# Kernel optimization log

Hardware: AMD Instinct MI355X
Metric: run time of the kernel (lower is better)

## Reference

```python
import jax, jax.numpy as jnp
import numpy as np

N, D, H, E, K = 4096, 512, 2048, 8, 2  # tokens, input/output dim, expert hidden, num_experts, top_k


def setup_inputs() -> dict:
    key = jax.random.key(0)
    k_x, k_r, k_w1, k_b1, k_w2, k_b2 = jax.random.split(key, 6)
    input_batch = jax.random.normal(k_x, (N, D), dtype=jnp.float32)
    # Router-style top-k selection: guarantees the K expert ids per token are distinct
    # (required by the torch nonzero-based dispatch) and probabilities are a softmax
    # over the selected logits, matching a standard MoE sampler.
    router_logits = jax.random.normal(k_r, (N, E), dtype=jnp.float32)
    top_vals, top_idx = jax.lax.top_k(router_logits, K)
    probabilities = jax.nn.softmax(top_vals, axis=-1)            # [N, K]
    indices = top_idx.astype(jnp.int64)                          # [N, K]
    scale = 0.02
    W1 = scale * jax.random.normal(k_w1, (E, D, H), dtype=jnp.float32)
    b1 = jnp.zeros((E, H), dtype=jnp.float32)
    W2 = scale * jax.random.normal(k_w2, (E, H, D), dtype=jnp.float32)
    b2 = jnp.zeros((E, D), dtype=jnp.float32)
    return {"input_batch": input_batch, "probabilities": probabilities, "indices": indices,
            "W1": W1, "b1": b1, "W2": W2, "b2": b2}


def reference(input_batch, probabilities, indices, W1, b1, W2, b2):
    # Each expert is a dense 2-layer GELU MLP. The torch module gathers the tokens
    # assigned to each expert, runs the expert, concatenates, sorts back to original
    # flattened [N*K] order, applies probability weighting AFTER the experts, then
    # reshapes to [N, K, D] and sums over K. That is mathematically:
    #   out[t] = sum_k probabilities[t, k] * expert_{indices[t, k]}(input_batch[t])
    h = jax.nn.gelu(jnp.einsum('nd,edh->enh', input_batch, W1) + b1[:, None, :])  # [E, N, H]
    y = jnp.einsum('enh,ehd->end', h, W2) + b2[:, None, :]                         # [E, N, D]
    y = jnp.transpose(y, (1, 0, 2))                                                # [N, E, D]
    sel = jnp.take_along_axis(y, indices[:, :, None], axis=1)                      # [N, K, D]
    output = jnp.sum(sel * probabilities[:, :, None], axis=1)                      # [N, D]
    total_loss = jnp.float32(0.0)  # no sampler / expert aux losses in this config
    return output, total_loss
```

## Files before the change

kernel.cpp:

```cpp
#include <hip/hip_runtime.h>
#include <cstdint>
#include <cstddef>

#define NTOK 4096
#define DIMD 512
#define HIDH 2048
#define NEXP 8
#define TOPK 2
#define NSLOT (NTOK*TOPK)
#define SLACK 256
#define YROWS (NSLOT+SLACK)

#define BK 64

typedef short bf16x8_t __attribute__((ext_vector_type(8)));
typedef float f32x4_t  __attribute__((ext_vector_type(4)));

__device__ __forceinline__ unsigned short f2b(float f){
  unsigned int x = __float_as_uint(f);
  unsigned int r = (x + 0x7FFFu + ((x >> 16) & 1u)) >> 16;
  return (unsigned short)r;
}

__device__ __forceinline__ float gelu_tanh(float x) {
  float z2 = 1.5957691216057308f * fmaf(0.044715f * x, x * x, x);
  return x / (1.f + __expf(-z2));
}

__device__ __forceinline__ void gl_lds16(const void* g, void* l){
  __builtin_amdgcn_global_load_lds((const __attribute__((address_space(1))) void*)g,
                                   (__attribute__((address_space(3))) void*)l, 16, 0, 0);
}


__global__ __launch_bounds__(256) void cvt_x(const float* __restrict__ x, unsigned short* __restrict__ xb){
  int i = blockIdx.x*256 + threadIdx.x;
  if (i >= (NTOK*DIMD)/4) return;
  float4 v = ((const float4*)x)[i];
  ushort4 o; o.x=f2b(v.x); o.y=f2b(v.y); o.z=f2b(v.z); o.w=f2b(v.w);
  ((ushort4*)xb)[i] = o;
}

__global__ __launch_bounds__(256) void transpose_cvt(const float* __restrict__ src,
                                                     unsigned short* __restrict__ dst,
                                                     int R, int C){
  int e = blockIdx.z;
  src += (size_t)e*R*C; dst += (size_t)e*R*C;
  int c0 = blockIdx.x*64, r0 = blockIdx.y*64;
  __shared__ float t[64][65];
  int tr = threadIdx.x >> 4, tc = threadIdx.x & 15;
  #pragma unroll
  for (int i=0;i<4;i++){
    int r = tr + i*16;
    float4 v = *(const float4*)(src + (size_t)(r0 + r)*C + c0 + tc*4);
    t[r][tc*4+0]=v.x; t[r][tc*4+1]=v.y; t[r][tc*4+2]=v.z; t[r][tc*4+3]=v.w;
  }
  __syncthreads();
  #pragma unroll
  for (int i=0;i<4;i++){
    int c = tr + i*16;
    ushort4 o;
    o.x = f2b(t[tc*4+0][c]); o.y = f2b(t[tc*4+1][c]);
    o.z = f2b(t[tc*4+2][c]); o.w = f2b(t[tc*4+3][c]);
    *(ushort4*)(dst + (size_t)(c0 + c)*R + r0 + tc*4) = o;
  }
}


__global__ void count_k(const int* __restrict__ I, int* __restrict__ meta){
  int i = blockIdx.x*256+threadIdx.x;
  if (i < NSLOT) atomicAdd(&meta[I[i]], 1);
}
__global__ void scan_k(int* __restrict__ meta){
  if (threadIdx.x==0 && blockIdx.x==0){
    int s=0;
    for(int e=0;e<NEXP;e++){ meta[16+e]=s; s+=meta[e]; }
  }
}
__global__ void fill_k(const int* __restrict__ I, int* __restrict__ meta,
                       int* __restrict__ tokOf, int* __restrict__ rowOf){
  int i = blockIdx.x*256+threadIdx.x;
  if (i < NSLOT){
    int e = I[i];
    int pos = meta[16+e] + atomicAdd(&meta[8+e], 1);
    tokOf[pos] = i >> 1;
    rowOf[i] = pos;
  }
}



__global__ __launch_bounds__(512,1) void gemm1(
    const unsigned short* __restrict__ Xb, const unsigned short* __restrict__ W1t,
    const float* __restrict__ B1, const int* __restrict__ meta,
    const int* __restrict__ tokOf, unsigned short* __restrict__ H)
{
  const int e = blockIdx.z;
  const int cnt = meta[e];
  const int row0 = blockIdx.y * 256;
  if (row0 >= cnt) return;
  const int off = meta[16+e];
  const int h0 = blockIdx.x * 256;

  extern __shared__ unsigned short sm[];

  const int tid = threadIdx.x;
  const int tr  = tid >> 3;
  const int csw = ((tid & 7) ^ (tr & 7)) << 3;

  const unsigned short* sA[4];
  const unsigned short* sB[4];
  #pragma unroll
  for (int i=0;i<4;i++){
    int slot = min(off + row0 + i*64 + tr, NSLOT-1);
    sA[i] = Xb  + (size_t)tokOf[slot]*DIMD + csw;
    sB[i] = W1t + ((size_t)e*HIDH + h0 + i*64 + tr)*DIMD + csw;
  }

  const int lane = tid & 63, wid = tid >> 6;
  const int wrM = (wid >> 2) * 128, wcN = (wid & 3) * 64;
  const int l15 = lane & 15, kg = lane >> 4;
  const int lx  = l15 & 7;
  int rowA[8], rowB[4];
  #pragma unroll
  for (int m=0;m<8;m++) rowA[m] = (wrM + m*16 + l15) * BK;
  #pragma unroll
  for (int n=0;n<4;n++) rowB[n] = (wcN + n*16 + l15) * BK;
  const int ch0 = ((kg    ) ^ lx) << 3;
  const int ch1 = ((kg + 4) ^ lx) << 3;

  f32x4_t acc[8][4];
  #pragma unroll
  for (int m=0;m<8;m++){
    #pragma unroll
    for (int n=0;n<4;n++) acc[m][n] = (f32x4_t){0.f,0.f,0.f,0.f};
  }

  auto stagef = [&](int buf, int kt){
    unsigned short* dA = sm + buf*32768 + tid*8;
    unsigned short* dB = dA + 16384;
    const int k0 = kt * BK;
    #pragma unroll
    for (int i=0;i<4;i++){
      gl_lds16(sA[i] + k0, dA + i*4096);
      gl_lds16(sB[i] + k0, dB + i*4096);
    }
  };

  auto khalf = [&](const unsigned short* SA, const unsigned short* SB, int ch){
    bf16x8_t bfr[4];
    #pragma unroll
    for (int n=0;n<4;n++) bfr[n] = *(const bf16x8_t*)&SB[rowB[n] + ch];
    #pragma unroll
    for (int m=0;m<8;m++){
      bf16x8_t afm = *(const bf16x8_t*)&SA[rowA[m] + ch];
      #pragma unroll
      for (int n=0;n<4;n++)
        acc[m][n] = __builtin_amdgcn_mfma_f32_16x16x32_bf16(afm, bfr[n], acc[m][n], 0,0,0);
    }
  };

  constexpr int NS = DIMD / BK;
  stagef(0, 0);
  for (int t = 0; t < NS; ++t){
    const int cur = t & 1;
    if (t + 1 < NS){
      stagef(cur ^ 1, t + 1);
      asm volatile("s_waitcnt vmcnt(8)" ::: "memory");
    } else {
      asm volatile("s_waitcnt vmcnt(0)" ::: "memory");
    }
    __builtin_amdgcn_s_barrier();
    __builtin_amdgcn_s_setprio(1);
    const unsigned short* SA = sm + cur*32768;
    const unsigned short* SB = SA + 16384;
    khalf(SA, SB, ch0);
    khalf(SA, SB, ch1);
    __builtin_amdgcn_s_setprio(0);
    __builtin_amdgcn_s_barrier();
  }

  const int r4 = kg * 4;
  #pragma unroll
  for (int n=0;n<4;n++){
    const int gcol = h0 + wcN + n*16 + l15;
    const float b1v = B1[(size_t)e*HIDH + gcol];
    #pragma unroll
    for (int m=0;m<8;m++){
      const int rbase = row0 + wrM + m*16 + r4;
      #pragma unroll
      for (int r=0;r<4;r++){
        const int row = rbase + r;
        if (row < cnt)
          H[(size_t)(off + row)*HIDH + gcol] = f2b(gelu_tanh(acc[m][n][r] + b1v));
      }
    }
  }
}


__global__ __launch_bounds__(512,1) void gemm2(
    const unsigned short* __restrict__ Hb, const unsigned short* __restrict__ W2t,
    const int* __restrict__ meta, float* __restrict__ Y, int nsplit)
{
  const int e = blockIdx.z;
  const int cnt = meta[e];
  const int row0 = blockIdx.y * 256;
  if (row0 >= cnt) return;
  const int off = meta[16+e];
  const int ncol = DIMD / 256;
  const int d0 = (blockIdx.x % ncol) * 256;
  const int kc = blockIdx.x / ncol;
  const int kchunk = HIDH / nsplit;
  const int kbase = kc * kchunk;
  const int NS = kchunk / BK;

  extern __shared__ unsigned short sm[];

  const int tid = threadIdx.x;
  const int tr  = tid >> 3;
  const int csw = ((tid & 7) ^ (tr & 7)) << 3;

  const unsigned short* sA[4];
  const unsigned short* sB[4];
  #pragma unroll
  for (int i=0;i<4;i++){
    int arow = min(off + row0 + i*64 + tr, YROWS-1);
    sA[i] = Hb  + (size_t)arow*HIDH + kbase + csw;
    sB[i] = W2t + ((size_t)e*DIMD + d0 + i*64 + tr)*HIDH + kbase + csw;
  }

  const int lane = tid & 63, wid = tid >> 6;
  const int wrM = (wid >> 2) * 128, wcN = (wid & 3) * 64;
  const int l15 = lane & 15, kg = lane >> 4;
  const int lx  = l15 & 7;
  int rowA[8], rowB[4];
  #pragma unroll
  for (int m=0;m<8;m++) rowA[m] = (wrM + m*16 + l15) * BK;
  #pragma unroll
  for (int n=0;n<4;n++) rowB[n] = (wcN + n*16 + l15) * BK;
  const int ch0 = ((kg    ) ^ lx) << 3;
  const int ch1 = ((kg + 4) ^ lx) << 3;

  f32x4_t acc[8][4];
  #pragma unroll
  for (int m=0;m<8;m++){
    #pragma unroll
    for (int n=0;n<4;n++) acc[m][n] = (f32x4_t){0.f,0.f,0.f,0.f};
  }

  auto stagef = [&](int buf, int kt){
    unsigned short* dA = sm + buf*32768 + tid*8;
    unsigned short* dB = dA + 16384;
    const int k0 = kt * BK;
    #pragma unroll
    for (int i=0;i<4;i++){
      gl_lds16(sA[i] + k0, dA + i*4096);
      gl_lds16(sB[i] + k0, dB + i*4096);
    }
  };

  auto khalf = [&](const unsigned short* SA, const unsigned short* SB, int ch){
    bf16x8_t bfr[4];
    #pragma unroll
    for (int n=0;n<4;n++) bfr[n] = *(const bf16x8_t*)&SB[rowB[n] + ch];
    #pragma unroll
    for (int m=0;m<8;m++){
      bf16x8_t afm = *(const bf16x8_t*)&SA[rowA[m] + ch];
      #pragma unroll
      for (int n=0;n<4;n++)
        acc[m][n] = __builtin_amdgcn_mfma_f32_16x16x32_bf16(afm, bfr[n], acc[m][n], 0,0,0);
    }
  };

  stagef(0, 0);
  for (int t = 0; t < NS; ++t){
    const int cur = t & 1;
    if (t + 1 < NS){
      stagef(cur ^ 1, t + 1);
      asm volatile("s_waitcnt vmcnt(8)" ::: "memory");
    } else {
      asm volatile("s_waitcnt vmcnt(0)" ::: "memory");
    }
    __builtin_amdgcn_s_barrier();
    __builtin_amdgcn_s_setprio(1);
    const unsigned short* SA = sm + cur*32768;
    const unsigned short* SB = SA + 16384;
    khalf(SA, SB, ch0);
    khalf(SA, SB, ch1);
    __builtin_amdgcn_s_setprio(0);
    __builtin_amdgcn_s_barrier();
  }

  float* Yp = Y + (size_t)kc * YROWS * DIMD;
  const int r4 = kg * 4;
  #pragma unroll
  for (int m=0;m<8;m++){
    const int rbase = row0 + wrM + m*16 + r4;
    #pragma unroll
    for (int r=0;r<4;r++){
      const int row = rbase + r;
      if (row < cnt){
        float* yp = Yp + (size_t)(off + row)*DIMD + d0 + wcN + l15;
        #pragma unroll
        for (int n=0;n<4;n++) yp[n*16] = acc[m][n][r];
      }
    }
  }
}


__global__ __launch_bounds__(128) void reduce_k(
    const float* __restrict__ P, const int* __restrict__ I, const int* __restrict__ rowOf,
    const float* __restrict__ Y, const float* __restrict__ B2, float* __restrict__ out,
    int nsplit)
{
  int t = blockIdx.x; int d4 = threadIdx.x;
  float4 a = make_float4(0.f,0.f,0.f,0.f);
  #pragma unroll
  for (int k=0;k<TOPK;k++){
    int i = t*TOPK + k;
    float p = P[i]; int e = I[i]; int r = rowOf[i];
    float4 b = *(const float4*)(B2 + (size_t)e*DIMD + d4*4);
    float4 y = make_float4(b.x, b.y, b.z, b.w);
    for (int c=0;c<nsplit;c++){
      float4 v = *(const float4*)(Y + (size_t)c*YROWS*DIMD + (size_t)r*DIMD + d4*4);
      y.x += v.x; y.y += v.y; y.z += v.z; y.w += v.w;
    }
    a.x = fmaf(p, y.x, a.x); a.y = fmaf(p, y.y, a.y);
    a.z = fmaf(p, y.z, a.z); a.w = fmaf(p, y.w, a.w);
  }
  *(float4*)(out + (size_t)t*DIMD + d4*4) = a;
}


#define CAP (NTOK*TOPK)
#define ROWS 32
#define HC 64
#define NTHR 256
#define XS_LD 516
#define HS_LD 36

__global__ void fb_build(const int* __restrict__ idx, const float* __restrict__ probs,
                         int* __restrict__ counts, int* __restrict__ tok,
                         float* __restrict__ pr) {
    int i = blockIdx.x * blockDim.x + threadIdx.x;
    if (i >= NTOK * TOPK) return;
    int t = i / TOPK;
    int e = idx[i];
    float p = probs[i];
    int pos = atomicAdd(&counts[e], 1);
    tok[e * CAP + pos] = t;
    pr[e * CAP + pos] = p;
}

__global__ __launch_bounds__(NTHR)
void fb_moe(const float* __restrict__ X,
            const float* __restrict__ W1, const float* __restrict__ B1,
            const float* __restrict__ W2, const float* __restrict__ B2,
            const int* __restrict__ counts, const int* __restrict__ tok,
            const float* __restrict__ pr, float* __restrict__ out)
{
    const int e = blockIdx.y;
    const int cnt = counts[e];
    const int r0 = blockIdx.x * ROWS;
    if (r0 >= cnt) return;
    const int nr = min(ROWS, cnt - r0);

    extern __shared__ float smem[];
    float* Xs = smem;
    float* Hs = smem + ROWS * XS_LD;
    const int tid = threadIdx.x;

    for (int i = tid; i < ROWS * (DIMD / 4); i += NTHR) {
        int r = i >> 7;
        int c4 = i & 127;
        float4 v = make_float4(0.f, 0.f, 0.f, 0.f);
        if (r < nr) {
            int t = tok[e * CAP + r0 + r];
            v = *(const float4*)(X + (size_t)t * DIMD + c4 * 4);
        }
        *(float4*)(Xs + r * XS_LD + c4 * 4) = v;
    }
    __syncthreads();

    const int hq = tid & 15;
    const int rp = tid >> 4;
    const int wv = tid >> 6;
    const int ln = tid & 63;

    float yacc[8][8];
    #pragma unroll
    for (int r = 0; r < 8; ++r){
        #pragma unroll
        for (int c = 0; c < 8; ++c) yacc[r][c] = 0.f;
    }

    const float* w1base = W1 + (size_t)e * DIMD * HIDH;
    const float* w2base = W2 + (size_t)e * HIDH * DIMD;
    const float* b1base = B1 + e * HIDH;

    for (int h0 = 0; h0 < HIDH; h0 += HC) {
        float acc0[4] = {0.f, 0.f, 0.f, 0.f};
        float acc1[4] = {0.f, 0.f, 0.f, 0.f};
        const float* w1p = w1base + h0 + hq * 4;
        const float* xr0 = Xs + (rp * 2) * XS_LD;
        const float* xr1 = xr0 + XS_LD;
        #pragma unroll 2
        for (int d = 0; d < DIMD; d += 4) {
            float4 xa = *(const float4*)(xr0 + d);
            float4 xb = *(const float4*)(xr1 + d);
            float4 w0 = *(const float4*)(w1p + (size_t)(d + 0) * HIDH);
            float4 w1v = *(const float4*)(w1p + (size_t)(d + 1) * HIDH);
            float4 w2v = *(const float4*)(w1p + (size_t)(d + 2) * HIDH);
            float4 w3v = *(const float4*)(w1p + (size_t)(d + 3) * HIDH);
            float xav[4] = {xa.x, xa.y, xa.z, xa.w};
            float xbv[4] = {xb.x, xb.y, xb.z, xb.w};
            float4 wsv[4] = {w0, w1v, w2v, w3v};
            #pragma unroll
            for (int dd = 0; dd < 4; ++dd) {
                acc0[0] = fmaf(xav[dd], wsv[dd].x, acc0[0]);
                acc0[1] = fmaf(xav[dd], wsv[dd].y, acc0[1]);
                acc0[2] = fmaf(xav[dd], wsv[dd].z, acc0[2]);
                acc0[3] = fmaf(xav[dd], wsv[dd].w, acc0[3]);
                acc1[0] = fmaf(xbv[dd], wsv[dd].x, acc1[0]);
                acc1[1] = fmaf(xbv[dd], wsv[dd].y, acc1[1]);
                acc1[2] = fmaf(xbv[dd], wsv[dd].z, acc1[2]);
                acc1[3] = fmaf(xbv[dd], wsv[dd].w, acc1[3]);
            }
        }
        {
            float4 b1v = *(const float4*)(b1base + h0 + hq * 4);
            float bb[4] = {b1v.x, b1v.y, b1v.z, b1v.w};
            #pragma unroll
            for (int j = 0; j < 4; ++j) {
                Hs[(hq * 4 + j) * HS_LD + rp * 2]     = gelu_tanh(acc0[j] + bb[j]);
                Hs[(hq * 4 + j) * HS_LD + rp * 2 + 1] = gelu_tanh(acc1[j] + bb[j]);
            }
        }
        __syncthreads();

        const float* w2p = w2base + (size_t)h0 * DIMD;
        #pragma unroll 4
        for (int hc = 0; hc < HC; ++hc) {
            float4 wA = *(const float4*)(w2p + (size_t)hc * DIMD + ln * 4);
            float4 wB = *(const float4*)(w2p + (size_t)hc * DIMD + 256 + ln * 4);
            float4 hv0 = *(const float4*)(Hs + hc * HS_LD + wv * 8);
            float4 hv1 = *(const float4*)(Hs + hc * HS_LD + wv * 8 + 4);
            float hr[8] = {hv0.x, hv0.y, hv0.z, hv0.w, hv1.x, hv1.y, hv1.z, hv1.w};
            #pragma unroll
            for (int r = 0; r < 8; ++r) {
                yacc[r][0] = fmaf(hr[r], wA.x, yacc[r][0]);
                yacc[r][1] = fmaf(hr[r], wA.y, yacc[r][1]);
                yacc[r][2] = fmaf(hr[r], wA.z, yacc[r][2]);
                yacc[r][3] = fmaf(hr[r], wA.w, yacc[r][3]);
                yacc[r][4] = fmaf(hr[r], wB.x, yacc[r][4]);
                yacc[r][5] = fmaf(hr[r], wB.y, yacc[r][5]);
                yacc[r][6] = fmaf(hr[r], wB.z, yacc[r][6]);
                yacc[r][7] = fmaf(hr[r], wB.w, yacc[r][7]);
            }
        }
        __syncthreads();
    }

    const float* b2p = B2 + e * DIMD;
    float4 b2A = *(const float4*)(b2p + ln * 4);
    float4 b2B = *(const float4*)(b2p + 256 + ln * 4);
    float bA[4] = {b2A.x, b2A.y, b2A.z, b2A.w};
    float bB[4] = {b2B.x, b2B.y, b2B.z, b2B.w};
    #pragma unroll
    for (int r = 0; r < 8; ++r) {
        int rg = wv * 8 + r;
        if (rg < nr) {
            int t = tok[e * CAP + r0 + rg];
            float p = pr[e * CAP + r0 + rg];
            float* op = out + (size_t)t * DIMD;
            #pragma unroll
            for (int j = 0; j < 4; ++j) {
                atomicAdd(op + ln * 4 + j,        p * (yacc[r][j] + bA[j]));
                atomicAdd(op + 256 + ln * 4 + j,  p * (yacc[r][4 + j] + bB[j]));
            }
        }
    }
}


extern "C" void kernel_launch(void* const* d_in, const int* in_sizes, int n_in,
                              void* d_out, int out_size, void* d_ws, size_t ws_size,
                              hipStream_t stream) {
    const float* X  = (const float*)d_in[0];
    const float* P  = (const float*)d_in[1];
    const int*   I  = (const int*)d_in[2];
    const float* W1 = (const float*)d_in[3];
    const float* B1 = (const float*)d_in[4];
    const float* W2 = (const float*)d_in[5];
    const float* B2 = (const float*)d_in[6];
    float* out = (float*)d_out;
    char* ws = (char*)d_ws;

    int nsplit = 0;
    size_t o_meta=0, o_tok=0, o_row=0, o_xb=0, o_w1t=0, o_w2t=0, o_h=0, o_y=0;
    const int cand[3] = {4, 2, 1};
    for (int ci = 0; ci < 3; ++ci) {
        int ns = cand[ci];
        size_t cur = 0;
        auto alloc = [&](size_t b){ size_t p = cur; cur += (b + 255) & ~(size_t)255; return p; };
        size_t m_ = alloc(256);
        size_t t_ = alloc((size_t)NSLOT*4);
        size_t r_ = alloc((size_t)NSLOT*4);
        size_t x_ = alloc((size_t)NTOK*DIMD*2);
        size_t w1_ = alloc((size_t)NEXP*DIMD*HIDH*2);
        size_t w2_ = alloc((size_t)NEXP*DIMD*HIDH*2);
        size_t h_ = alloc((size_t)YROWS*HIDH*2);
        size_t y_ = alloc((size_t)ns*YROWS*DIMD*4);
        if (cur <= ws_size) {
            nsplit = ns;
            o_meta=m_; o_tok=t_; o_row=r_; o_xb=x_; o_w1t=w1_; o_w2t=w2_; o_h=h_; o_y=y_;
            break;
        }
    }

    if (nsplit > 0) {
        int* meta = (int*)(ws + o_meta);
        int* tokOf = (int*)(ws + o_tok);
        int* rowOf = (int*)(ws + o_row);
        unsigned short* Xb  = (unsigned short*)(ws + o_xb);
        unsigned short* W1t = (unsigned short*)(ws + o_w1t);
        unsigned short* W2t = (unsigned short*)(ws + o_w2t);
        unsigned short* Hb  = (unsigned short*)(ws + o_h);
        float* Yb = (float*)(ws + o_y);

        hipMemsetAsync(meta, 0, 256, stream);
        cvt_x<<<(NTOK*DIMD/4 + 255)/256, 256, 0, stream>>>(X, Xb);
        transpose_cvt<<<dim3(HIDH/64, DIMD/64, NEXP), 256, 0, stream>>>(W1, W1t, DIMD, HIDH);
        transpose_cvt<<<dim3(DIMD/64, HIDH/64, NEXP), 256, 0, stream>>>(W2, W2t, HIDH, DIMD);
        count_k<<<NSLOT/256, 256, 0, stream>>>(I, meta);
        scan_k<<<1, 64, 0, stream>>>(meta);
        fill_k<<<NSLOT/256, 256, 0, stream>>>(I, meta, tokOf, rowOf);

        hipFuncSetAttribute((const void*)gemm1,
                            hipFuncAttributeMaxDynamicSharedMemorySize, 131072);
        hipFuncSetAttribute((const void*)gemm2,
                            hipFuncAttributeMaxDynamicSharedMemorySize, 131072);
        gemm1<<<dim3(HIDH/256, NSLOT/256, NEXP), 512, 131072, stream>>>(
            Xb, W1t, B1, meta, tokOf, Hb);
        gemm2<<<dim3((DIMD/256)*nsplit, NSLOT/256, NEXP), 512, 131072, stream>>>(
            Hb, W2t, meta, Yb, nsplit);
        reduce_k<<<NTOK, 128, 0, stream>>>(P, I, rowOf, Yb, B2, out, nsplit);
    } else {
        int*   counts = (int*)ws;
        int*   tok    = (int*)(ws + 64);
        float* pr     = (float*)(ws + 64 + (size_t)NEXP * CAP * sizeof(int));

        hipMemsetAsync(counts, 0, NEXP * sizeof(int), stream);
        hipMemsetAsync(d_out, 0, (size_t)out_size * sizeof(float), stream);
        fb_build<<<(NTOK * TOPK + 255) / 256, 256, 0, stream>>>(I, P, counts, tok, pr);
        size_t smem = (size_t)(ROWS * XS_LD + HC * HS_LD) * sizeof(float);
        hipFuncSetAttribute((const void*)fb_moe,
                            hipFuncAttributeMaxDynamicSharedMemorySize, (int)smem);
        fb_moe<<<dim3(CAP / ROWS, NEXP), NTHR, smem, stream>>>(
            X, W1, B1, W2, B2, counts, tok, pr, out);
    }
}
```

Measured before the change: 231.7 us.

## Shrink grouped GEMM tiles to 128x128 with 256 threads and two blocks per CU

Both expert GEMMs move from 256x256 tiles with 512 threads and one block per CU to 128x128 tiles with 256 threads, four waves and two blocks per CU, halving shared memory per block. The hand-tuned vmcnt waits, setprio hints and split barriers are replaced by a plain double-buffered loop with __syncthreads. The goal is more blocks and less padding waste on ragged per-expert row counts, plus better occupancy. In exchange each tile reuses loaded data less, and the simpler synchronisation may expose load latency.

Result: faster. 203.5 us (-12.2%).

```diff
diff --git a/kernel.cpp b/kernel.cpp
--- a/kernel.cpp
+++ b/kernel.cpp
@@ -11,7 +11,7 @@
 #define SLACK 256
 #define YROWS (NSLOT+SLACK)
 
-#define BK 64
+#define BK2 64
 
 typedef short bf16x8_t __attribute__((ext_vector_type(8)));
 typedef float f32x4_t  __attribute__((ext_vector_type(4)));
@@ -90,17 +90,17 @@
 
 
 
-__global__ __launch_bounds__(512,1) void gemm1(
+__global__ __launch_bounds__(256,2) void gemm1(
     const unsigned short* __restrict__ Xb, const unsigned short* __restrict__ W1t,
     const float* __restrict__ B1, const int* __restrict__ meta,
     const int* __restrict__ tokOf, unsigned short* __restrict__ H)
 {
   const int e = blockIdx.z;
   const int cnt = meta[e];
-  const int row0 = blockIdx.y * 256;
+  const int row0 = blockIdx.y * 128;
   if (row0 >= cnt) return;
   const int off = meta[16+e];
-  const int h0 = blockIdx.x * 256;
+  const int h0 = blockIdx.x * 128;
 
   extern __shared__ unsigned short sm[];
 
@@ -112,82 +112,76 @@
   const unsigned short* sB[4];
   #pragma unroll
   for (int i=0;i<4;i++){
-    int slot = min(off + row0 + i*64 + tr, NSLOT-1);
+    int slot = min(off + row0 + i*32 + tr, NSLOT-1);
     sA[i] = Xb  + (size_t)tokOf[slot]*DIMD + csw;
-    sB[i] = W1t + ((size_t)e*HIDH + h0 + i*64 + tr)*DIMD + csw;
+    sB[i] = W1t + ((size_t)e*HIDH + h0 + i*32 + tr)*DIMD + csw;
   }
 
   const int lane = tid & 63, wid = tid >> 6;
-  const int wrM = (wid >> 2) * 128, wcN = (wid & 3) * 64;
+  const int wr = (wid >> 1) * 64, wc = (wid & 1) * 64;
   const int l15 = lane & 15, kg = lane >> 4;
-  const int lx  = l15 & 7;
-  int rowA[8], rowB[4];
-  #pragma unroll
-  for (int m=0;m<8;m++) rowA[m] = (wrM + m*16 + l15) * BK;
-  #pragma unroll
-  for (int n=0;n<4;n++) rowB[n] = (wcN + n*16 + l15) * BK;
-  const int ch0 = ((kg    ) ^ lx) << 3;
-  const int ch1 = ((kg + 4) ^ lx) << 3;
-
-  f32x4_t acc[8][4];
-  #pragma unroll
-  for (int m=0;m<8;m++){
-    #pragma unroll
-    for (int n=0;n<4;n++) acc[m][n] = (f32x4_t){0.f,0.f,0.f,0.f};
-  }
-
-  auto stagef = [&](int buf, int kt){
-    unsigned short* dA = sm + buf*32768 + tid*8;
-    unsigned short* dB = dA + 16384;
-    const int k0 = kt * BK;
+  int rowA[4], rowB[4];
+  #pragma unroll
+  for (int m=0;m<4;m++) rowA[m] = (wr + m*16 + l15) * BK2;
+  #pragma unroll
+  for (int n=0;n<4;n++) rowB[n] = (wc + n*16 + l15) * BK2;
+  const int ch0 = ((kg    ) ^ (l15 & 7)) << 3;
+  const int ch1 = ((kg + 4) ^ (l15 & 7)) << 3;
+
+  f32x4_t acc[4][4];
+  #pragma unroll
+  for (int i=0;i<4;i++){
+    #pragma unroll
+    for (int j=0;j<4;j++) acc[i][j] = (f32x4_t){0.f,0.f,0.f,0.f};
+  }
+
+  auto stage = [&](int buf, int kt){
+    unsigned short* d = sm + buf*16384 + tid*8;
+    const int k0 = kt * BK2;
     #pragma unroll
     for (int i=0;i<4;i++){
-      gl_lds16(sA[i] + k0, dA + i*4096);
-      gl_lds16(sB[i] + k0, dB + i*4096);
+      gl_lds16(sA[i] + k0, d + i*2048);
+      gl_lds16(sB[i] + k0, d + 8192 + i*2048);
     }
   };
 
-  auto khalf = [&](const unsigned short* SA, const unsigned short* SB, int ch){
-    bf16x8_t bfr[4];
-    #pragma unroll
-    for (int n=0;n<4;n++) bfr[n] = *(const bf16x8_t*)&SB[rowB[n] + ch];
-    #pragma unroll
-    for (int m=0;m<8;m++){
-      bf16x8_t afm = *(const bf16x8_t*)&SA[rowA[m] + ch];
-      #pragma unroll
-      for (int n=0;n<4;n++)
-        acc[m][n] = __builtin_amdgcn_mfma_f32_16x16x32_bf16(afm, bfr[n], acc[m][n], 0,0,0);
+  auto compute = [&](int buf){
+    const unsigned short* SA = sm + buf*16384;
+    const unsigned short* SB = SA + 8192;
+    #pragma unroll
+    for (int h=0; h<2; ++h){
+      const int ch = h ? ch1 : ch0;
+      bf16x8_t bfr[4], af[4];
+      #pragma unroll
+      for (int n=0;n<4;n++) bfr[n] = *(const bf16x8_t*)&SB[rowB[n] + ch];
+      #pragma unroll
+      for (int m=0;m<4;m++) af[m]  = *(const bf16x8_t*)&SA[rowA[m] + ch];
+      #pragma unroll
+      for (int m=0;m<4;m++){
+        #pragma unroll
+        for (int n=0;n<4;n++)
+          acc[m][n] = __builtin_amdgcn_mfma_f32_16x16x32_bf16(af[m], bfr[n], acc[m][n], 0,0,0);
+      }
     }
   };
 
-  constexpr int NS = DIMD / BK;
-  stagef(0, 0);
+  constexpr int NS = DIMD / BK2;
+  stage(0, 0);
+  __syncthreads();
   for (int t = 0; t < NS; ++t){
-    const int cur = t & 1;
-    if (t + 1 < NS){
-      stagef(cur ^ 1, t + 1);
-      asm volatile("s_waitcnt vmcnt(8)" ::: "memory");
-    } else {
-      asm volatile("s_waitcnt vmcnt(0)" ::: "memory");
-    }
-    __builtin_amdgcn_s_barrier();
-    __builtin_amdgcn_s_setprio(1);
-    const unsigned short* SA = sm + cur*32768;
-    const unsigned short* SB = SA + 16384;
-    khalf(SA, SB, ch0);
-    khalf(SA, SB, ch1);
-    __builtin_amdgcn_s_setprio(0);
-    __builtin_amdgcn_s_barrier();
+    if (t + 1 < NS) stage((t+1) & 1, t+1);
+    compute(t & 1);
+    __syncthreads();
   }
 
   const int r4 = kg * 4;
   #pragma unroll
   for (int n=0;n<4;n++){
-    const int gcol = h0 + wcN + n*16 + l15;
+    const int gcol = h0 + wc + n*16 + l15;
     const float b1v = B1[(size_t)e*HIDH + gcol];
     #pragma unroll
-    for (int m=0;m<8;m++){
-      const int rbase = row0 + wrM + m*16 + r4;
+    for (int m=0;m<4;m++){
+      const int rbase = row0 + wr + m*16 + r4;
       #pragma unroll
       for (int r=0;r<4;r++){
         const int row = rbase + r;
@@ -199,21 +193,21 @@
 }
 
 
-__global__ __launch_bounds__(512,1) void gemm2(
+__global__ __launch_bounds__(256,2) void gemm2(
     const unsigned short* __restrict__ Hb, const unsigned short* __restrict__ W2t,
     const int* __restrict__ meta, float* __restrict__ Y, int nsplit)
 {
   const int e = blockIdx.z;
   const int cnt = meta[e];
-  const int row0 = blockIdx.y * 256;
+  const int row0 = blockIdx.y * 128;
   if (row0 >= cnt) return;
   const int off = meta[16+e];
-  const int ncol = DIMD / 256;
-  const int d0 = (blockIdx.x % ncol) * 256;
+  const int ncol = DIMD / 128;
+  const int d0 = (blockIdx.x % ncol) * 128;
   const int kc = blockIdx.x / ncol;
   const int kchunk = HIDH / nsplit;
   const int kbase = kc * kchunk;
-  const int NS = kchunk / BK;
+  const int NS = kchunk / BK2;
 
   extern __shared__ unsigned short sm[];
 
@@ -225,83 +219,77 @@
   const unsigned short* sB[4];
   #pragma unroll
   for (int i=0;i<4;i++){
-    int arow = min(off + row0 + i*64 + tr, YROWS-1);
+    int arow = min(off + row0 + i*32 + tr, YROWS-1);
     sA[i] = Hb  + (size_t)arow*HIDH + kbase + csw;
-    sB[i] = W2t + ((size_t)e*DIMD + d0 + i*64 + tr)*HIDH + kbase + csw;
+    sB[i] = W2t + ((size_t)e*DIMD + d0 + i*32 + tr)*HIDH + kbase + csw;
   }
 
   const int lane = tid & 63, wid = tid >> 6;
-  const int wrM = (wid >> 2) * 128, wcN = (wid & 3) * 64;
+  const int wr = (wid >> 1) * 64, wc = (wid & 1) * 64;
   const int l15 = lane & 15, kg = lane >> 4;
-  const int lx  = l15 & 7;
-  int rowA[8], rowB[4];
-  #pragma unroll
-  for (int m=0;m<8;m++) rowA[m] = (wrM + m*16 + l15) * BK;
-  #pragma unroll
-  for (int n=0;n<4;n++) rowB[n] = (wcN + n*16 + l15) * BK;
-  const int ch0 = ((kg    ) ^ lx) << 3;
-  const int ch1 = ((kg + 4) ^ lx) << 3;
-
-  f32x4_t acc[8][4];
-  #pragma unroll
-  for (int m=0;m<8;m++){
-    #pragma unroll
-    for (int n=0;n<4;n++) acc[m][n] = (f32x4_t){0.f,0.f,0.f,0.f};
-  }
-
-  auto stagef = [&](int buf, int kt){
-    unsigned short* dA = sm + buf*32768 + tid*8;
-    unsigned short* dB = dA + 16384;
-    const int k0 = kt * BK;
+  int rowA[4], rowB[4];
+  #pragma unroll
+  for (int m=0;m<4;m++) rowA[m] = (wr + m*16 + l15) * BK2;
+  #pragma unroll
+  for (int n=0;n<4;n++) rowB[n] = (wc + n*16 + l15) * BK2;
+  const int ch0 = ((kg    ) ^ (l15 & 7)) << 3;
+  const int ch1 = ((kg + 4) ^ (l15 & 7)) << 3;
+
+  f32x4_t acc[4][4];
+  #pragma unroll
+  for (int i=0;i<4;i++){
+    #pragma unroll
+    for (int j=0;j<4;j++) acc[i][j] = (f32x4_t){0.f,0.f,0.f,0.f};
+  }
+
+  auto stage = [&](int buf, int kt){
+    unsigned short* d = sm + buf*16384 + tid*8;
+    const int k0 = kt * BK2;
     #pragma unroll
     for (int i=0;i<4;i++){
-      gl_lds16(sA[i] + k0, dA + i*4096);
-      gl_lds16(sB[i] + k0, dB + i*4096);
+      gl_lds16(sA[i] + k0, d + i*2048);
+      gl_lds16(sB[i] + k0, d + 8192 + i*2048);
     }
   };
 
-  auto khalf = [&](const unsigned short* SA, const unsigned short* SB, int ch){
-    bf16x8_t bfr[4];
-    #pragma unroll
-    for (int n=0;n<4;n++) bfr[n] = *(const bf16x8_t*)&SB[rowB[n] + ch];
-    #pragma unroll
-    for (int m=0;m<8;m++){
-      bf16x8_t afm = *(const bf16x8_t*)&SA[rowA[m] + ch];
-      #pragma unroll
-      for (int n=0;n<4;n++)
-        acc[m][n] = __builtin_amdgcn_mfma_f32_16x16x32_bf16(afm, bfr[n], acc[m][n], 0,0,0);
+  auto compute = [&](int buf){
+    const unsigned short* SA = sm + buf*16384;
+    const unsigned short* SB = SA + 8192;
+    #pragma unroll
+    for (int h=0; h<2; ++h){
+      const int ch = h ? ch1 : ch0;
+      bf16x8_t bfr[4], af[4];
+      #pragma unroll
+      for (int n=0;n<4;n++) bfr[n] = *(const bf16x8_t*)&SB[rowB[n] + ch];
+      #pragma unroll
+      for (int m=0;m<4;m++) af[m]  = *(const bf16x8_t*)&SA[rowA[m] + ch];
+      #pragma unroll
+      for (int m=0;m<4;m++){
+        #pragma unroll
+        for (int n=0;n<4;n++)
+          acc[m][n] = __builtin_amdgcn_mfma_f32_16x16x32_bf16(af[m], bfr[n], acc[m][n], 0,0,0);
+      }
     }
   };
 
-  stagef(0, 0);
+  stage(0, 0);
+  __syncthreads();
   for (int t = 0; t < NS; ++t){
-    const int cur = t & 1;
-    if (t + 1 < NS){
-      stagef(cur ^ 1, t + 1);
-      asm volatile("s_waitcnt vmcnt(8)" ::: "memory");
-    } else {
-      asm volatile("s_waitcnt vmcnt(0)" ::: "memory");
-    }
-    __builtin_amdgcn_s_barrier();
-    __builtin_amdgcn_s_setprio(1);
-    const unsigned short* SA = sm + cur*32768;
-    const unsigned short* SB = SA + 16384;
-    khalf(SA, SB, ch0);
-    khalf(SA, SB, ch1);
-    __builtin_amdgcn_s_setprio(0);
-    __builtin_amdgcn_s_barrier();
+    if (t + 1 < NS) stage((t+1) & 1, t+1);
+    compute(t & 1);
+    __syncthreads();
   }
 
   float* Yp = Y + (size_t)kc * YROWS * DIMD;
   const int r4 = kg * 4;
   #pragma unroll
-  for (int m=0;m<8;m++){
-    const int rbase = row0 + wrM + m*16 + r4;
+  for (int m=0;m<4;m++){
+    const int rbase = row0 + wr + m*16 + r4;
     #pragma unroll
     for (int r=0;r<4;r++){
       const int row = rbase + r;
       if (row < cnt){
-        float* yp = Yp + (size_t)(off + row)*DIMD + d0 + wcN + l15;
+        float* yp = Yp + (size_t)(off + row)*DIMD + d0 + wc + l15;
         #pragma unroll
         for (int n=0;n<4;n++) yp[n*16] = acc[m][n][r];
       }
@@ -539,12 +527,12 @@
         fill_k<<<NSLOT/256, 256, 0, stream>>>(I, meta, tokOf, rowOf);
 
         hipFuncSetAttribute((const void*)gemm1,
-                            hipFuncAttributeMaxDynamicSharedMemorySize, 131072);
+                            hipFuncAttributeMaxDynamicSharedMemorySize, 65536);
         hipFuncSetAttribute((const void*)gemm2,
-                            hipFuncAttributeMaxDynamicSharedMemorySize, 131072);
-        gemm1<<<dim3(HIDH/256, NSLOT/256, NEXP), 512, 131072, stream>>>(
+                            hipFuncAttributeMaxDynamicSharedMemorySize, 65536);
+        gemm1<<<dim3(HIDH/128, NSLOT/128, NEXP), 256, 65536, stream>>>(
             Xb, W1t, B1, meta, tokOf, Hb);
-        gemm2<<<dim3((DIMD/256)*nsplit, NSLOT/256, NEXP), 512, 131072, stream>>>(
+        gemm2<<<dim3((DIMD/128)*nsplit, NSLOT/128, NEXP), 256, 65536, stream>>>(
             Hb, W2t, meta, Yb, nsplit);
         reduce_k<<<NTOK, 128, 0, stream>>>(P, I, rowOf, Yb, B2, out, nsplit);
     } else {
```
